# Performance work log

Measured on AMD Instinct MI355X. Metric: run time of the kernel, lower is better.

## Reference

```python
import jax, jax.numpy as jnp
import numpy as np

N = 100000       # nodes
E = 3200000      # edges (avg degree 32)
NFEAT = 500
NHID = 256
NCLASS = 40
NLAYERS = 5
EPS = 1e-5


def layer_norm(x, g, b):
    mu = jnp.mean(x, axis=-1, keepdims=True)
    var = jnp.mean(jnp.square(x - mu), axis=-1, keepdims=True)
    return (x - mu) * jax.lax.rsqrt(var + EPS) * g + b


def spmm(row, col, val, x):
    # out[i] = sum_{e: row[e]==i} val[e] * x[col[e]]  == adj @ x
    return jax.ops.segment_sum(val[:, None] * x[col], row, num_segments=N)


def setup_inputs() -> dict:
    key = jax.random.key(0)
    ks = jax.random.split(key, 10)
    s_in = 1.0 / np.sqrt(NFEAT)
    s_h = 1.0 / np.sqrt(NHID)
    return {
        "x": jax.random.normal(ks[0], (N, NFEAT), jnp.float32),
        "row": jax.random.randint(ks[1], (E,), 0, N, jnp.int32),
        "col": jax.random.randint(ks[2], (E,), 0, N, jnp.int32),
        "val": jax.random.uniform(ks[3], (E,), jnp.float32) * (1.0 / 32.0),
        "in_W": jax.random.normal(ks[4], (NHID, NFEAT), jnp.float32) * s_in,
        "in_b": jnp.zeros((NHID,), jnp.float32),
        "convW": jax.random.normal(ks[5], (NLAYERS, NHID, NHID), jnp.float32) * s_h,
        "convB": jnp.zeros((NLAYERS, NHID), jnp.float32),
        "lnG": jnp.ones((NLAYERS, NHID), jnp.float32),
        "lnB": jnp.zeros((NLAYERS, NHID), jnp.float32),
        "outG": jnp.ones((NHID,), jnp.float32),
        "outB": jnp.zeros((NHID,), jnp.float32),
        "out_W": jax.random.normal(ks[6], (NCLASS, NHID), jnp.float32) * s_h,
        "out_b": jnp.zeros((NCLASS,), jnp.float32),
        "only_z": 1,
    }


def reference(x, row, col, val, in_W, in_b, convW, convB, lnG, lnB,
              outG, outB, out_W, out_b, only_z):
    # input layer (input_dropout=0, so dropout is identity)
    h = jax.nn.relu(x @ in_W.T + in_b)
    # residual GCN layers with pre-LayerNorm (norm['flag'] == True)
    for i in range(NLAYERS):
        r = layer_norm(h, lnG[i], lnB[i])
        r = spmm(row, col, val, r)          # sparse aggregation
        r = r @ convW[i].T + convB[i]       # single linear (n_linear=1)
        if i < NLAYERS - 1:                 # last conv has last_layer=True -> no act
            r = jax.nn.relu(r)
        h = h + r
    mid = h                                 # captured at i == n_layers-1 (post-residual)
    z = layer_norm(h, outG, outB) @ out_W.T + out_b  # squeeze(1) is a no-op for nclass=40
    if only_z:
        return z
    return (mid, z)
```

## Files before the change

kernel.cpp:

```cpp
#include <hip/hip_runtime.h>
#include <stdint.h>

#define NFEAT 500
#define KPAD  512
#define NHID  256
#define NCLS  40
#define NCPAD 48
#define NLAY  5
#define BSH   8
#define CHUNK 8192

typedef __attribute__((ext_vector_type(8))) short short8;
typedef __attribute__((ext_vector_type(4))) float f32x4;

__device__ __forceinline__ ushort f2bf(float f) {
  uint32_t u = __float_as_uint(f);
  u += 0x7fffu + ((u >> 16) & 1u);
  return (ushort)(u >> 16);
}
__device__ __forceinline__ float b2f(ushort h) {
  return __uint_as_float(((uint32_t)h) << 16);
}

__global__ __launch_bounds__(256) void k_cast_pad(const float* __restrict__ src,
    ushort* __restrict__ dst, int rows, int scol, int dcol) {
  int id = blockIdx.x * 256 + threadIdx.x;
  int cpr = dcol >> 2;
  if (id >= rows * cpr) return;
  int r = id / cpr;
  int c = (id % cpr) * 4;
  float4 v;
  if (c + 3 < scol) {
    v = *(const float4*)(src + (size_t)r * scol + c);
  } else {
    v.x = (c + 0 < scol) ? src[(size_t)r * scol + c + 0] : 0.f;
    v.y = (c + 1 < scol) ? src[(size_t)r * scol + c + 1] : 0.f;
    v.z = (c + 2 < scol) ? src[(size_t)r * scol + c + 2] : 0.f;
    v.w = (c + 3 < scol) ? src[(size_t)r * scol + c + 3] : 0.f;
  }
  ushort4 o;
  o.x = f2bf(v.x); o.y = f2bf(v.y); o.z = f2bf(v.z); o.w = f2bf(v.w);
  *(ushort4*)(dst + (size_t)r * dcol + c) = o;
}

__global__ __launch_bounds__(256) void kA_scatter(const int* __restrict__ row,
    const int* __restrict__ col, const float* __restrict__ val,
    int* __restrict__ ccur, int2* __restrict__ pb, int E, int P, int CAP) {
  __shared__ int lh[512];
  const int t = threadIdx.x;
  const int b0 = blockIdx.x * CHUNK;
  for (int i = t; i < P; i += 256) lh[i] = 0;
  __syncthreads();
#pragma unroll 4
  for (int i = 0; i < CHUNK / 256; i++) {
    int idx = b0 + i * 256 + t;
    if (idx < E) atomicAdd(&lh[row[idx] >> BSH], 1);
  }
  __syncthreads();
  for (int i = t; i < P; i += 256) {
    int c = lh[i];
    lh[i] = (c > 0) ? atomicAdd(&ccur[i], c) : 0;
  }
  __syncthreads();
#pragma unroll 4
  for (int i = 0; i < CHUNK / 256; i++) {
    int idx = b0 + i * 256 + t;
    if (idx < E) {
      int r = row[idx];
      int p = r >> BSH;
      int pos = atomicAdd(&lh[p], 1);
      if (pos < CAP)
        pb[(size_t)p * CAP + pos] =
            make_int2(col[idx] | ((r & 255) << 24), __float_as_int(val[idx]));
    }
  }
}

__global__ __launch_bounds__(256) void kB_cnt(const int* __restrict__ ccur,
    const int2* __restrict__ pb, int* __restrict__ cnt, int* __restrict__ bsum,
    int N, int CAP) {
  __shared__ int lc[256];
  __shared__ int ws[4];
  const int b = blockIdx.x;
  const int t = threadIdx.x;
  lc[t] = 0;
  __syncthreads();
  int cb = min(ccur[b], CAP);
  size_t base = (size_t)b * CAP;
  for (int i = t; i < cb; i += 256)
    atomicAdd(&lc[((uint32_t)pb[base + i].x) >> 24], 1);
  __syncthreads();
  int c = lc[t];
  int r = (b << BSH) + t;
  if (r < N) cnt[r] = c;
  int v = c;
  v += __shfl_xor(v, 1); v += __shfl_xor(v, 2); v += __shfl_xor(v, 4);
  v += __shfl_xor(v, 8); v += __shfl_xor(v, 16); v += __shfl_xor(v, 32);
  if ((t & 63) == 0) ws[t >> 6] = v;
  __syncthreads();
  if (t == 0) bsum[b] = ws[0] + ws[1] + ws[2] + ws[3];
}

__global__ __launch_bounds__(1024) void k_scanP(const int* __restrict__ bsum,
    int* __restrict__ boff, int* __restrict__ ptrN, int P) {
  __shared__ int ls[1024];
  int t = threadIdx.x;
  int v = (t < P) ? bsum[t] : 0;
  ls[t] = v;
  __syncthreads();
  for (int off = 1; off < 1024; off <<= 1) {
    int u = (t >= off) ? ls[t - off] : 0;
    __syncthreads();
    ls[t] += u;
    __syncthreads();
  }
  if (t < P) boff[t] = ls[t] - v;
  if (t == 1023) *ptrN = ls[1023];
}

__global__ __launch_bounds__(256) void kB_ptr(const int* __restrict__ cnt,
    const int* __restrict__ boff, int* __restrict__ ptr, int N) {
  __shared__ int ls[256];
  int b = blockIdx.x;
  int t = threadIdx.x;
  int r = (b << BSH) + t;
  int v = (r < N) ? cnt[r] : 0;
  ls[t] = v;
  __syncthreads();
  for (int off = 1; off < 256; off <<= 1) {
    int u = (t >= off) ? ls[t - off] : 0;
    __syncthreads();
    ls[t] += u;
    __syncthreads();
  }
  if (r < N) ptr[r] = boff[b] + ls[t] - v;
}

__global__ __launch_bounds__(256) void kB_scatter(const int* __restrict__ ccur,
    const int2* __restrict__ pb, const int* __restrict__ ptr,
    int2* __restrict__ cv, int CAP) {
  __shared__ int rk[256];
  const int b = blockIdx.x;
  rk[threadIdx.x] = 0;
  __syncthreads();
  int cb = min(ccur[b], CAP);
  size_t base = (size_t)b * CAP;
  for (int i = threadIdx.x; i < cb; i += 256) {
    int2 p2 = pb[base + i];
    int r8 = ((uint32_t)p2.x) >> 24;
    int r = (b << BSH) + r8;
    int rank = atomicAdd(&rk[r8], 1);
    cv[ptr[r] + rank] = make_int2(p2.x & 0x00FFFFFF, p2.y);
  }
}

template<int FP8OUT>
__global__ __launch_bounds__(256) void k_ln(const ushort* __restrict__ h,
    const float* __restrict__ g, const float* __restrict__ b,
    void* __restrict__ o, int n) {
  int r = (blockIdx.x * 256 + threadIdx.x) >> 6;
  int lane = threadIdx.x & 63;
  if (r >= n) return;
  ushort4 hv = *(const ushort4*)(h + (size_t)r * NHID + lane * 4);
  float v0 = b2f(hv.x), v1 = b2f(hv.y), v2 = b2f(hv.z), v3 = b2f(hv.w);
  float s = v0 + v1 + v2 + v3;
  s += __shfl_xor(s, 1); s += __shfl_xor(s, 2); s += __shfl_xor(s, 4);
  s += __shfl_xor(s, 8); s += __shfl_xor(s, 16); s += __shfl_xor(s, 32);
  float mu = s * (1.f / NHID);
  float d0 = v0 - mu, d1 = v1 - mu, d2 = v2 - mu, d3 = v3 - mu;
  float q = d0 * d0 + d1 * d1 + d2 * d2 + d3 * d3;
  q += __shfl_xor(q, 1); q += __shfl_xor(q, 2); q += __shfl_xor(q, 4);
  q += __shfl_xor(q, 8); q += __shfl_xor(q, 16); q += __shfl_xor(q, 32);
  float rs = rsqrtf(q * (1.f / NHID) + 1e-5f);
  float4 gv = *(const float4*)(g + lane * 4);
  float4 bv = *(const float4*)(b + lane * 4);
  float o0 = d0 * rs * gv.x + bv.x;
  float o1 = d1 * rs * gv.y + bv.y;
  float o2 = d2 * rs * gv.z + bv.z;
  float o3 = d3 * rs * gv.w + bv.w;
  if (FP8OUT) {
    int w = 0;
    w = __builtin_amdgcn_cvt_pk_fp8_f32(o0, o1, w, false);
    w = __builtin_amdgcn_cvt_pk_fp8_f32(o2, o3, w, true);
    ((uint32_t*)o)[(size_t)r * 64 + lane] = (uint32_t)w;
  } else {
    ushort4 t;
    t.x = f2bf(o0); t.y = f2bf(o1); t.z = f2bf(o2); t.w = f2bf(o3);
    *(ushort4*)((ushort*)o + (size_t)r * NHID + lane * 4) = t;
  }
}

__global__ __launch_bounds__(256) void k_spmm(const int* __restrict__ ptr,
    const int2* __restrict__ cv, const uint32_t* __restrict__ t8,
    ushort* __restrict__ agg, int n) {
  int r = (blockIdx.x * 256 + threadIdx.x) >> 6;
  int lane = threadIdx.x & 63;
  if (r >= n) return;
  int s = ptr[r], e = ptr[r + 1];
  int cnt = e - s;
  int q = lane >> 4;
  int seg = lane & 15;
  float acc[16];
#pragma unroll
  for (int j = 0; j < 16; j++) acc[j] = 0.f;

  for (int base = 0; base < cnt; base += 64) {
    int idx = s + base + lane;
    int ec = 0; float ev = 0.f;
    if (idx < e) {
      int2 p2 = cv[idx];
      ec = p2.x;
      ev = __uint_as_float((uint32_t)p2.y);
    }
    int lim = min(64, cnt - base);
#pragma unroll 2
    for (int i = 0; i < lim; i += 4) {
      int a = i + q;
      int c = __shfl(ec, a);
      float v = __shfl(ev, a);
      uint4 tv = *(const uint4*)(t8 + (size_t)c * 64 + seg * 4);
      auto p0 = __builtin_amdgcn_cvt_pk_f32_fp8(tv.x, false);
      auto p1 = __builtin_amdgcn_cvt_pk_f32_fp8(tv.x, true);
      auto p2 = __builtin_amdgcn_cvt_pk_f32_fp8(tv.y, false);
      auto p3 = __builtin_amdgcn_cvt_pk_f32_fp8(tv.y, true);
      auto p4 = __builtin_amdgcn_cvt_pk_f32_fp8(tv.z, false);
      auto p5 = __builtin_amdgcn_cvt_pk_f32_fp8(tv.z, true);
      auto p6 = __builtin_amdgcn_cvt_pk_f32_fp8(tv.w, false);
      auto p7 = __builtin_amdgcn_cvt_pk_f32_fp8(tv.w, true);
      acc[0]  += v * p0[0]; acc[1]  += v * p0[1];
      acc[2]  += v * p1[0]; acc[3]  += v * p1[1];
      acc[4]  += v * p2[0]; acc[5]  += v * p2[1];
      acc[6]  += v * p3[0]; acc[7]  += v * p3[1];
      acc[8]  += v * p4[0]; acc[9]  += v * p4[1];
      acc[10] += v * p5[0]; acc[11] += v * p5[1];
      acc[12] += v * p6[0]; acc[13] += v * p6[1];
      acc[14] += v * p7[0]; acc[15] += v * p7[1];
    }
  }

#pragma unroll
  for (int j = 0; j < 16; j++) {
    acc[j] += __shfl_xor(acc[j], 16);
    acc[j] += __shfl_xor(acc[j], 32);
  }
  if (q == 0) {
    short8 o0, o1;
#pragma unroll
    for (int j = 0; j < 8; j++) { o0[j] = (short)f2bf(acc[j]); o1[j] = (short)f2bf(acc[8 + j]); }
    *(short8*)(agg + (size_t)r * NHID + seg * 16) = o0;
    *(short8*)(agg + (size_t)r * NHID + seg * 16 + 8) = o1;
  }
}

template<int MODE>
__global__ __launch_bounds__(256) void k_gemm(const ushort* __restrict__ A,
    const ushort* __restrict__ B, const float* __restrict__ bias,
    ushort* __restrict__ H, int M, int K) {
  __shared__ ushort As[128 * 32];
  __shared__ ushort Bs[128 * 32];
  const int t = threadIdx.x;
  const int lane = t & 63;
  const int wid = t >> 6;
  const int brow = blockIdx.x * 128;
  const int bcol = blockIdx.y * 128;
  const int wr = (wid >> 1) * 64;
  const int wc = (wid & 1) * 64;
  const int l15 = lane & 15, hi = lane >> 4;
  const f32x4 z4 = {0.f, 0.f, 0.f, 0.f};
  f32x4 acc[4][4];
  for (int m = 0; m < 4; m++)
    for (int n = 0; n < 4; n++) acc[m][n] = z4;

  for (int k0 = 0; k0 < K; k0 += 32) {
    __syncthreads();
#pragma unroll
    for (int c = 0; c < 2; c++) {
      int s = c * 256 + t;
      int r = s >> 2;
      int kk = (s & 3) * 8;
      int gr = brow + r; gr = gr < M ? gr : M - 1;
      const ushort* ga = A + (size_t)gr * K + (k0 + kk);
      __builtin_amdgcn_global_load_lds((const __attribute__((address_space(1))) void*)ga,
          (__attribute__((address_space(3))) void*)(As + s * 8), 16, 0, 0);
      const ushort* gb = B + (size_t)(bcol + r) * K + (k0 + kk);
      __builtin_amdgcn_global_load_lds((const __attribute__((address_space(1))) void*)gb,
          (__attribute__((address_space(3))) void*)(Bs + s * 8), 16, 0, 0);
    }
    __syncthreads();
    short8 af[4], bf[4];
#pragma unroll
    for (int m = 0; m < 4; m++)
      af[m] = *(const short8*)(As + (wr + m * 16 + l15) * 32 + hi * 8);
#pragma unroll
    for (int n = 0; n < 4; n++)
      bf[n] = *(const short8*)(Bs + (wc + n * 16 + l15) * 32 + hi * 8);
#pragma unroll
    for (int m = 0; m < 4; m++)
#pragma unroll
      for (int n = 0; n < 4; n++)
        acc[m][n] = __builtin_amdgcn_mfma_f32_16x16x32_bf16(af[m], bf[n], acc[m][n], 0, 0, 0);
  }

#pragma unroll
  for (int m = 0; m < 4; m++) {
    int gr0 = brow + wr + m * 16 + hi * 4;
#pragma unroll
    for (int n = 0; n < 4; n++) {
      int gc = bcol + wc + n * 16 + l15;
      float bv = bias[gc];
#pragma unroll
      for (int j = 0; j < 4; j++) {
        int gr = gr0 + j;
        if (gr < M) {
          size_t idx = (size_t)gr * NHID + gc;
          float v = acc[m][n][j] + bv;
          if (MODE == 0)      H[idx] = f2bf(fmaxf(v, 0.f));
          else if (MODE == 1) H[idx] = f2bf(b2f(H[idx]) + fmaxf(v, 0.f));
          else                H[idx] = f2bf(b2f(H[idx]) + v);
        }
      }
    }
  }
}

__global__ __launch_bounds__(256) void k_ogemm(const ushort* __restrict__ A,
    const ushort* __restrict__ Bw, const float* __restrict__ ob,
    float* __restrict__ z, int M) {
  __shared__ ushort As[256 * 32];
  __shared__ ushort Bs[NCPAD * 264];
  const int t = threadIdx.x;
  const int lane = t & 63;
  const int wid = t >> 6;
  const int brow = blockIdx.x * 256;
  const int wr = wid * 64;
  const int l15 = lane & 15, hi = lane >> 4;
  const f32x4 z4 = {0.f, 0.f, 0.f, 0.f};
  f32x4 acc[4][3];
#pragma unroll
  for (int m = 0; m < 4; m++)
#pragma unroll
    for (int n = 0; n < 3; n++) acc[m][n] = z4;

  for (int i = t; i < NCPAD * 33; i += 256) {
    int r = i / 33, cc = i % 33;
    if (cc < 32)
      *(short8*)(Bs + r * 264 + cc * 8) = *(const short8*)(Bw + r * 256 + cc * 8);
  }

  for (int k0 = 0; k0 < 256; k0 += 32) {
    __syncthreads();
#pragma unroll
    for (int c = 0; c < 4; c++) {
      int s = c * 256 + t;
      int r = s >> 2;
      int kk = (s & 3) * 8;
      int gr = brow + r; gr = gr < M ? gr : M - 1;
      const ushort* ga = A + (size_t)gr * NHID + (k0 + kk);
      __builtin_amdgcn_global_load_lds((const __attribute__((address_space(1))) void*)ga,
          (__attribute__((address_space(3))) void*)(As + s * 8), 16, 0, 0);
    }
    __syncthreads();
    short8 af[4], bf[3];
#pragma unroll
    for (int m = 0; m < 4; m++)
      af[m] = *(const short8*)(As + (wr + m * 16 + l15) * 32 + hi * 8);
#pragma unroll
    for (int n = 0; n < 3; n++)
      bf[n] = *(const short8*)(Bs + (n * 16 + l15) * 264 + k0 + hi * 8);
#pragma unroll
    for (int m = 0; m < 4; m++)
#pragma unroll
      for (int n = 0; n < 3; n++)
        acc[m][n] = __builtin_amdgcn_mfma_f32_16x16x32_bf16(af[m], bf[n], acc[m][n], 0, 0, 0);
  }

#pragma unroll
  for (int m = 0; m < 4; m++) {
    int gr0 = brow + wr + m * 16 + hi * 4;
#pragma unroll
    for (int n = 0; n < 3; n++) {
      int gc = n * 16 + l15;
      if (gc < NCLS) {
        float bv = ob[gc];
#pragma unroll
        for (int j = 0; j < 4; j++) {
          int gr = gr0 + j;
          if (gr < M) z[(size_t)gr * NCLS + gc] = acc[m][n][j] + bv;
        }
      }
    }
  }
}

extern "C" void kernel_launch(void* const* d_in, const int* in_sizes, int n_in,
                              void* d_out, int out_size, void* d_ws, size_t ws_size,
                              hipStream_t stream) {
  const float* x     = (const float*)d_in[0];
  const int*   row   = (const int*)d_in[1];
  const int*   col   = (const int*)d_in[2];
  const float* val   = (const float*)d_in[3];
  const float* inW   = (const float*)d_in[4];
  const float* inB   = (const float*)d_in[5];
  const float* convW = (const float*)d_in[6];
  const float* convB = (const float*)d_in[7];
  const float* lnG   = (const float*)d_in[8];
  const float* lnB   = (const float*)d_in[9];
  const float* outG  = (const float*)d_in[10];
  const float* outB  = (const float*)d_in[11];
  const float* outW  = (const float*)d_in[12];
  const float* outb  = (const float*)d_in[13];
  const int N = in_sizes[0] / NFEAT;
  const int E = in_sizes[1];
  float* z = (float*)d_out;

  const int P   = (N + 255) >> BSH;
  const int CAP = ((((E + P - 1) / P) * 5 / 4 + 256) + 15) & ~15;

  char* wsp = (char*)d_ws;
  size_t off = 0;
  auto alloc = [&](size_t bytes) {
    void* p = wsp + off;
    off += (bytes + 255) & ~(size_t)255;
    return p;
  };
  ushort*   h   = (ushort*)alloc((size_t)N * NHID * 2);
  ushort*   tb  = (ushort*)alloc((size_t)N * NHID * 2);
  ushort*   ab  = (ushort*)alloc((size_t)N * NHID * 2);
  uint32_t* t8  = (uint32_t*)alloc((size_t)N * 64 * 4);
  ushort*   xb  = (ushort*)alloc((size_t)N * KPAD * 2);
  ushort*   wbi = (ushort*)alloc((size_t)NHID * KPAD * 2);
  ushort*   wbc = (ushort*)alloc((size_t)NLAY * NHID * NHID * 2);
  ushort*   wbo = (ushort*)alloc((size_t)NCPAD * NHID * 2);
  int*   cnt  = (int*)alloc((size_t)N * 4);
  int*   ptr  = (int*)alloc((size_t)(N + 1) * 4);
  int*   ccur = (int*)alloc((size_t)P * 4);
  int*   bsum = (int*)alloc((size_t)P * 4);
  int*   boff = (int*)alloc((size_t)P * 4);
  int2*  cv   = (int2*)alloc((size_t)E * 8);
  int2*  pb   = (int2*)xb;

  {
    int tot = N * (KPAD >> 2);
    k_cast_pad<<<(tot + 255) / 256, 256, 0, stream>>>(x, xb, N, NFEAT, KPAD);
    tot = NHID * (KPAD >> 2);
    k_cast_pad<<<(tot + 255) / 256, 256, 0, stream>>>(inW, wbi, NHID, NFEAT, KPAD);
    tot = NLAY * NHID * (NHID >> 2);
    k_cast_pad<<<(tot + 255) / 256, 256, 0, stream>>>(convW, wbc, NLAY * NHID, NHID, NHID);
    hipMemsetAsync(wbo, 0, (size_t)NCPAD * NHID * 2, stream);
    tot = NCLS * (NHID >> 2);
    k_cast_pad<<<(tot + 255) / 256, 256, 0, stream>>>(outW, wbo, NCLS, NHID, NHID);
  }

  dim3 gg((N + 127) / 128, NHID / 128);
  k_gemm<0><<<gg, 256, 0, stream>>>(xb, wbi, inB, h, N, KPAD);

  hipMemsetAsync(ccur, 0, (size_t)P * 4, stream);
  kA_scatter<<<(E + CHUNK - 1) / CHUNK, 256, 0, stream>>>(row, col, val, ccur, pb, E, P, CAP);
  kB_cnt<<<P, 256, 0, stream>>>(ccur, pb, cnt, bsum, N, CAP);
  k_scanP<<<1, 1024, 0, stream>>>(bsum, boff, ptr + N, P);
  kB_ptr<<<P, 256, 0, stream>>>(cnt, boff, ptr, N);
  kB_scatter<<<P, 256, 0, stream>>>(ccur, pb, ptr, cv, CAP);

  int nwb = (N + 3) / 4;
  for (int i = 0; i < NLAY; i++) {
    k_ln<1><<<nwb, 256, 0, stream>>>(h, lnG + i * NHID, lnB + i * NHID, t8, N);
    k_spmm<<<nwb, 256, 0, stream>>>(ptr, cv, t8, ab, N);
    if (i < NLAY - 1)
      k_gemm<1><<<gg, 256, 0, stream>>>(ab, wbc + (size_t)i * NHID * NHID,
                                        convB + i * NHID, h, N, NHID);
    else
      k_gemm<2><<<gg, 256, 0, stream>>>(ab, wbc + (size_t)i * NHID * NHID,
                                        convB + i * NHID, h, N, NHID);
  }

  k_ln<0><<<nwb, 256, 0, stream>>>(h, outG, outB, tb, N);
  k_ogemm<<<(N + 255) / 256, 256, 0, stream>>>(tb, wbo, outb, z, N);
}
```

Baseline: 1.259 ms.

## Fuse x cast into input GEMM, widen GEMM tiles to full 256 columns, pack spmm FMAs

The input GEMM now reads fp32 x directly, converting it to bf16 in registers while staging into LDS. This removes the separate cast/pad kernel and the padded bf16 copy of x. Both GEMMs now have each block cover all 256 output columns with 128 rows, so the A tile is loaded once instead of twice across a column-split grid. The spmm accumulators become 2-wide float vectors using elementwise FMA so the compiler can emit packed FMA. The costs are a larger register footprint (32 accumulator tiles per wave), more LDS for the B tile, and a separate allocation for the scatter buffer that used to alias xb.

```diff
diff --git a/kernel.cpp b/kernel.cpp
--- a/kernel.cpp
+++ b/kernel.cpp
@@ -12,6 +12,7 @@
 
 typedef __attribute__((ext_vector_type(8))) short short8;
 typedef __attribute__((ext_vector_type(4))) float f32x4;
+typedef __attribute__((ext_vector_type(2))) float f32x2;
 
 __device__ __forceinline__ ushort f2bf(float f) {
   uint32_t u = __float_as_uint(f);
@@ -200,9 +201,9 @@
   int cnt = e - s;
   int q = lane >> 4;
   int seg = lane & 15;
-  float acc[16];
-#pragma unroll
-  for (int j = 0; j < 16; j++) acc[j] = 0.f;
+  f32x2 acc2[8];
+#pragma unroll
+  for (int j = 0; j < 8; j++) acc2[j] = (f32x2){0.f, 0.f};
 
   for (int base = 0; base < cnt; base += 64) {
     int idx = s + base + lane;
@@ -218,95 +219,174 @@
       int a = i + q;
       int c = __shfl(ec, a);
       float v = __shfl(ev, a);
+      f32x2 vv = {v, v};
       uint4 tv = *(const uint4*)(t8 + (size_t)c * 64 + seg * 4);
-      auto p0 = __builtin_amdgcn_cvt_pk_f32_fp8(tv.x, false);
-      auto p1 = __builtin_amdgcn_cvt_pk_f32_fp8(tv.x, true);
-      auto p2 = __builtin_amdgcn_cvt_pk_f32_fp8(tv.y, false);
-      auto p3 = __builtin_amdgcn_cvt_pk_f32_fp8(tv.y, true);
-      auto p4 = __builtin_amdgcn_cvt_pk_f32_fp8(tv.z, false);
-      auto p5 = __builtin_amdgcn_cvt_pk_f32_fp8(tv.z, true);
-      auto p6 = __builtin_amdgcn_cvt_pk_f32_fp8(tv.w, false);
-      auto p7 = __builtin_amdgcn_cvt_pk_f32_fp8(tv.w, true);
-      acc[0]  += v * p0[0]; acc[1]  += v * p0[1];
-      acc[2]  += v * p1[0]; acc[3]  += v * p1[1];
-      acc[4]  += v * p2[0]; acc[5]  += v * p2[1];
-      acc[6]  += v * p3[0]; acc[7]  += v * p3[1];
-      acc[8]  += v * p4[0]; acc[9]  += v * p4[1];
-      acc[10] += v * p5[0]; acc[11] += v * p5[1];
-      acc[12] += v * p6[0]; acc[13] += v * p6[1];
-      acc[14] += v * p7[0]; acc[15] += v * p7[1];
-    }
-  }
-
+      f32x2 p;
+      p = __builtin_amdgcn_cvt_pk_f32_fp8(tv.x, false);
+      acc2[0] = __builtin_elementwise_fma(p, vv, acc2[0]);
+      p = __builtin_amdgcn_cvt_pk_f32_fp8(tv.x, true);
+      acc2[1] = __builtin_elementwise_fma(p, vv, acc2[1]);
+      p = __builtin_amdgcn_cvt_pk_f32_fp8(tv.y, false);
+      acc2[2] = __builtin_elementwise_fma(p, vv, acc2[2]);
+      p = __builtin_amdgcn_cvt_pk_f32_fp8(tv.y, true);
+      acc2[3] = __builtin_elementwise_fma(p, vv, acc2[3]);
+      p = __builtin_amdgcn_cvt_pk_f32_fp8(tv.z, false);
+      acc2[4] = __builtin_elementwise_fma(p, vv, acc2[4]);
+      p = __builtin_amdgcn_cvt_pk_f32_fp8(tv.z, true);
+      acc2[5] = __builtin_elementwise_fma(p, vv, acc2[5]);
+      p = __builtin_amdgcn_cvt_pk_f32_fp8(tv.w, false);
+      acc2[6] = __builtin_elementwise_fma(p, vv, acc2[6]);
+      p = __builtin_amdgcn_cvt_pk_f32_fp8(tv.w, true);
+      acc2[7] = __builtin_elementwise_fma(p, vv, acc2[7]);
+    }
+  }
+
+  float accs[16];
+#pragma unroll
+  for (int j = 0; j < 8; j++) { accs[2 * j] = acc2[j][0]; accs[2 * j + 1] = acc2[j][1]; }
 #pragma unroll
   for (int j = 0; j < 16; j++) {
-    acc[j] += __shfl_xor(acc[j], 16);
-    acc[j] += __shfl_xor(acc[j], 32);
+    accs[j] += __shfl_xor(accs[j], 16);
+    accs[j] += __shfl_xor(accs[j], 32);
   }
   if (q == 0) {
     short8 o0, o1;
 #pragma unroll
-    for (int j = 0; j < 8; j++) { o0[j] = (short)f2bf(acc[j]); o1[j] = (short)f2bf(acc[8 + j]); }
+    for (int j = 0; j < 8; j++) { o0[j] = (short)f2bf(accs[j]); o1[j] = (short)f2bf(accs[8 + j]); }
     *(short8*)(agg + (size_t)r * NHID + seg * 16) = o0;
     *(short8*)(agg + (size_t)r * NHID + seg * 16 + 8) = o1;
   }
 }
 
-template<int MODE>
-__global__ __launch_bounds__(256) void k_gemm(const ushort* __restrict__ A,
+__global__ __launch_bounds__(256) void k_gemm0(const float* __restrict__ X,
     const ushort* __restrict__ B, const float* __restrict__ bias,
-    ushort* __restrict__ H, int M, int K) {
+    ushort* __restrict__ H, int M) {
   __shared__ ushort As[128 * 32];
-  __shared__ ushort Bs[128 * 32];
+  __shared__ ushort Bs[256 * 32];
   const int t = threadIdx.x;
   const int lane = t & 63;
-  const int wid = t >> 6;
+  const int w = t >> 6;
   const int brow = blockIdx.x * 128;
-  const int bcol = blockIdx.y * 128;
-  const int wr = (wid >> 1) * 64;
-  const int wc = (wid & 1) * 64;
+  const int l15 = lane & 15, hi = lane >> 4;
+  const int ar = t >> 1, ah = (t & 1) * 16;
+  const int agr = min(brow + ar, M - 1);
+  const f32x4 z4 = {0.f, 0.f, 0.f, 0.f};
+  f32x4 acc[2][16];
+#pragma unroll
+  for (int m = 0; m < 2; m++)
+#pragma unroll
+    for (int n = 0; n < 16; n++) acc[m][n] = z4;
+
+  for (int k0 = 0; k0 < KPAD; k0 += 32) {
+    __syncthreads();
+    ushort av[16];
+#pragma unroll
+    for (int c = 0; c < 4; c++) {
+      int col = k0 + ah + c * 4;
+      float4 v = {0.f, 0.f, 0.f, 0.f};
+      if (col + 3 < NFEAT) v = *(const float4*)(X + (size_t)agr * NFEAT + col);
+      av[c * 4 + 0] = f2bf(v.x); av[c * 4 + 1] = f2bf(v.y);
+      av[c * 4 + 2] = f2bf(v.z); av[c * 4 + 3] = f2bf(v.w);
+    }
+#pragma unroll
+    for (int c = 0; c < 4; c++) {
+      int s = c * 256 + t;
+      int rr = s >> 2;
+      int kk = (s & 3) * 8;
+      const ushort* gb = B + (size_t)rr * KPAD + (k0 + kk);
+      __builtin_amdgcn_global_load_lds((const __attribute__((address_space(1))) void*)gb,
+          (__attribute__((address_space(3))) void*)(Bs + s * 8), 16, 0, 0);
+    }
+    *(short8*)(As + ar * 32 + ah) = *(short8*)av;
+    *(short8*)(As + ar * 32 + ah + 8) = *(short8*)(av + 8);
+    __syncthreads();
+    short8 af[2];
+#pragma unroll
+    for (int m = 0; m < 2; m++)
+      af[m] = *(const short8*)(As + (w * 32 + m * 16 + l15) * 32 + hi * 8);
+#pragma unroll
+    for (int n = 0; n < 16; n++) {
+      short8 bf = *(const short8*)(Bs + (n * 16 + l15) * 32 + hi * 8);
+      acc[0][n] = __builtin_amdgcn_mfma_f32_16x16x32_bf16(af[0], bf, acc[0][n], 0, 0, 0);
+      acc[1][n] = __builtin_amdgcn_mfma_f32_16x16x32_bf16(af[1], bf, acc[1][n], 0, 0, 0);
+    }
+  }
+
+#pragma unroll
+  for (int m = 0; m < 2; m++) {
+    int gr0 = brow + w * 32 + m * 16 + hi * 4;
+#pragma unroll
+    for (int n = 0; n < 16; n++) {
+      int gc = n * 16 + l15;
+      float bv = bias[gc];
+#pragma unroll
+      for (int j = 0; j < 4; j++) {
+        int gr = gr0 + j;
+        if (gr < M)
+          H[(size_t)gr * NHID + gc] = f2bf(fmaxf(acc[m][n][j] + bv, 0.f));
+      }
+    }
+  }
+}
+
+template<int MODE>
+__global__ __launch_bounds__(256) void k_gemmc(const ushort* __restrict__ A,
+    const ushort* __restrict__ B, const float* __restrict__ bias,
+    ushort* __restrict__ H, int M) {
+  __shared__ ushort As[128 * 32];
+  __shared__ ushort Bs[256 * 32];
+  const int t = threadIdx.x;
+  const int lane = t & 63;
+  const int w = t >> 6;
+  const int brow = blockIdx.x * 128;
   const int l15 = lane & 15, hi = lane >> 4;
   const f32x4 z4 = {0.f, 0.f, 0.f, 0.f};
-  f32x4 acc[4][4];
-  for (int m = 0; m < 4; m++)
-    for (int n = 0; n < 4; n++) acc[m][n] = z4;
-
-  for (int k0 = 0; k0 < K; k0 += 32) {
+  f32x4 acc[2][16];
+#pragma unroll
+  for (int m = 0; m < 2; m++)
+#pragma unroll
+    for (int n = 0; n < 16; n++) acc[m][n] = z4;
+
+  for (int k0 = 0; k0 < NHID; k0 += 32) {
     __syncthreads();
 #pragma unroll
     for (int c = 0; c < 2; c++) {
       int s = c * 256 + t;
-      int r = s >> 2;
+      int rr = s >> 2;
       int kk = (s & 3) * 8;
-      int gr = brow + r; gr = gr < M ? gr : M - 1;
-      const ushort* ga = A + (size_t)gr * K + (k0 + kk);
+      int gr = brow + rr; gr = gr < M ? gr : M - 1;
+      const ushort* ga = A + (size_t)gr * NHID + (k0 + kk);
       __builtin_amdgcn_global_load_lds((const __attribute__((address_space(1))) void*)ga,
           (__attribute__((address_space(3))) void*)(As + s * 8), 16, 0, 0);
-      const ushort* gb = B + (size_t)(bcol + r) * K + (k0 + kk);
+    }
+#pragma unroll
+    for (int c = 0; c < 4; c++) {
+      int s = c * 256 + t;
+      int rr = s >> 2;
+      int kk = (s & 3) * 8;
+      const ushort* gb = B + (size_t)rr * NHID + (k0 + kk);
       __builtin_amdgcn_global_load_lds((const __attribute__((address_space(1))) void*)gb,
           (__attribute__((address_space(3))) void*)(Bs + s * 8), 16, 0, 0);
     }
     __syncthreads();
-    short8 af[4], bf[4];
-#pragma unroll
-    for (int m = 0; m < 4; m++)
-      af[m] = *(const short8*)(As + (wr + m * 16 + l15) * 32 + hi * 8);
-#pragma unroll
-    for (int n = 0; n < 4; n++)
-      bf[n] = *(const short8*)(Bs + (wc + n * 16 + l15) * 32 + hi * 8);
-#pragma unroll
-    for (int m = 0; m < 4; m++)
-#pragma unroll
-      for (int n = 0; n < 4; n++)
-        acc[m][n] = __builtin_amdgcn_mfma_f32_16x16x32_bf16(af[m], bf[n], acc[m][n], 0, 0, 0);
-  }
-
-#pragma unroll
-  for (int m = 0; m < 4; m++) {
-    int gr0 = brow + wr + m * 16 + hi * 4;
-#pragma unroll
-    for (int n = 0; n < 4; n++) {
-      int gc = bcol + wc + n * 16 + l15;
+    short8 af[2];
+#pragma unroll
+    for (int m = 0; m < 2; m++)
+      af[m] = *(const short8*)(As + (w * 32 + m * 16 + l15) * 32 + hi * 8);
+#pragma unroll
+    for (int n = 0; n < 16; n++) {
+      short8 bf = *(const short8*)(Bs + (n * 16 + l15) * 32 + hi * 8);
+      acc[0][n] = __builtin_amdgcn_mfma_f32_16x16x32_bf16(af[0], bf, acc[0][n], 0, 0, 0);
+      acc[1][n] = __builtin_amdgcn_mfma_f32_16x16x32_bf16(af[1], bf, acc[1][n], 0, 0, 0);
+    }
+  }
+
+#pragma unroll
+  for (int m = 0; m < 2; m++) {
+    int gr0 = brow + w * 32 + m * 16 + hi * 4;
+#pragma unroll
+    for (int n = 0; n < 16; n++) {
+      int gc = n * 16 + l15;
       float bv = bias[gc];
 #pragma unroll
       for (int j = 0; j < 4; j++) {
@@ -314,9 +394,8 @@
         if (gr < M) {
           size_t idx = (size_t)gr * NHID + gc;
           float v = acc[m][n][j] + bv;
-          if (MODE == 0)      H[idx] = f2bf(fmaxf(v, 0.f));
-          else if (MODE == 1) H[idx] = f2bf(b2f(H[idx]) + fmaxf(v, 0.f));
-          else                H[idx] = f2bf(b2f(H[idx]) + v);
+          if (MODE == 1) H[idx] = f2bf(b2f(H[idx]) + fmaxf(v, 0.f));
+          else           H[idx] = f2bf(b2f(H[idx]) + v);
         }
       }
     }
@@ -427,7 +506,6 @@
   ushort*   tb  = (ushort*)alloc((size_t)N * NHID * 2);
   ushort*   ab  = (ushort*)alloc((size_t)N * NHID * 2);
   uint32_t* t8  = (uint32_t*)alloc((size_t)N * 64 * 4);
-  ushort*   xb  = (ushort*)alloc((size_t)N * KPAD * 2);
   ushort*   wbi = (ushort*)alloc((size_t)NHID * KPAD * 2);
   ushort*   wbc = (ushort*)alloc((size_t)NLAY * NHID * NHID * 2);
   ushort*   wbo = (ushort*)alloc((size_t)NCPAD * NHID * 2);
@@ -437,12 +515,10 @@
   int*   bsum = (int*)alloc((size_t)P * 4);
   int*   boff = (int*)alloc((size_t)P * 4);
   int2*  cv   = (int2*)alloc((size_t)E * 8);
-  int2*  pb   = (int2*)xb;
+  int2*  pb   = (int2*)alloc((size_t)P * CAP * 8);
 
   {
-    int tot = N * (KPAD >> 2);
-    k_cast_pad<<<(tot + 255) / 256, 256, 0, stream>>>(x, xb, N, NFEAT, KPAD);
-    tot = NHID * (KPAD >> 2);
+    int tot = NHID * (KPAD >> 2);
     k_cast_pad<<<(tot + 255) / 256, 256, 0, stream>>>(inW, wbi, NHID, NFEAT, KPAD);
     tot = NLAY * NHID * (NHID >> 2);
     k_cast_pad<<<(tot + 255) / 256, 256, 0, stream>>>(convW, wbc, NLAY * NHID, NHID, NHID);
@@ -451,8 +527,9 @@
     k_cast_pad<<<(tot + 255) / 256, 256, 0, stream>>>(outW, wbo, NCLS, NHID, NHID);
   }
 
-  dim3 gg((N + 127) / 128, NHID / 128);
-  k_gemm<0><<<gg, 256, 0, stream>>>(xb, wbi, inB, h, N, KPAD);
+  const int ng = (N + 127) / 128;
+
+  k_gemm0<<<ng, 256, 0, stream>>>(x, wbi, inB, h, N);
 
   hipMemsetAsync(ccur, 0, (size_t)P * 4, stream);
   kA_scatter<<<(E + CHUNK - 1) / CHUNK, 256, 0, stream>>>(row, col, val, ccur, pb, E, P, CAP);
@@ -466,11 +543,11 @@
     k_ln<1><<<nwb, 256, 0, stream>>>(h, lnG + i * NHID, lnB + i * NHID, t8, N);
     k_spmm<<<nwb, 256, 0, stream>>>(ptr, cv, t8, ab, N);
     if (i < NLAY - 1)
-      k_gemm<1><<<gg, 256, 0, stream>>>(ab, wbc + (size_t)i * NHID * NHID,
-                                        convB + i * NHID, h, N, NHID);
+      k_gemmc<1><<<ng, 256, 0, stream>>>(ab, wbc + (size_t)i * NHID * NHID,
+                                         convB + i * NHID, h, N);
     else
-      k_gemm<2><<<gg, 256, 0, stream>>>(ab, wbc + (size_t)i * NHID * NHID,
-                                        convB + i * NHID, h, N, NHID);
+      k_gemmc<2><<<ng, 256, 0, stream>>>(ab, wbc + (size_t)i * NHID * NHID,
+                                         convB + i * NHID, h, N);
   }
 
   k_ln<0><<<nwb, 256, 0, stream>>>(h, outG, outB, tb, N);
```

Measured after the change: 1.635 ms. 1.3x slower.
